# Performance work log

Measured on AMD Instinct MI355X. Metric: run time of the kernel, lower is better.

Reference implementation:

```python
import jax, jax.numpy as jnp
import numpy as np

E, T, D, H = 32, 65536, 512, 1024


def setup_inputs() -> dict:
    key = jax.random.key(0)
    k = jax.random.split(key, 7)
    norm = lambda kk, shp, sc: (jax.random.normal(kk, shp, jnp.float32) * sc)
    x = norm(k[0], (T, D), 1.0)
    w1 = norm(k[1], (E, D, H), D ** -0.5)   # per-expert up-proj (gate branch)
    b1 = norm(k[2], (E, H), 0.02)
    w3 = norm(k[3], (E, D, H), D ** -0.5)   # per-expert up-proj (linear branch)
    b3 = norm(k[4], (E, H), 0.02)
    w2 = norm(k[5], (E, H, D), H ** -0.5)   # per-expert down-proj
    b2 = norm(k[6], (E, D), 0.02)
    # tokens are pre-sorted by expert; uniform dispatch of T//E tokens per expert
    group_sizes = jnp.full((E,), T // E, jnp.int32)
    return dict(x=x, w1=w1, b1=b1, w3=w3, b3=b3, w2=w2, b2=b2,
                group_sizes=group_sizes)


def reference(x, w1, b1, w3, b3, w2, b2, group_sizes):
    # expert id per token, derived from contiguous group sizes
    bounds = jnp.cumsum(group_sizes)                       # [E]
    seg = jnp.searchsorted(bounds, jnp.arange(x.shape[0]), side='right')  # [T]
    # grouped GEMMs: per-expert weight bank applied to its contiguous token slab
    h1 = jax.lax.ragged_dot(x, w1, group_sizes) + b1[seg]  # [T,H]
    h3 = jax.lax.ragged_dot(x, w3, group_sizes) + b3[seg]  # [T,H]
    h = jax.nn.silu(h1) * h3                               # SwiGLU gate
    out = jax.lax.ragged_dot(h, w2, group_sizes) + b2[seg] # [T,D]
    return out
```

## Files before the change

### kernel.cpp

```cpp
#include <hip/hip_runtime.h>
#include <hip/hip_bf16.h>

#define TOK 65536
#define NE  32
#define DD  512
#define HH  1024
#define TPE 2048

typedef short s16x8  __attribute__((ext_vector_type(8)));
typedef float f32x16 __attribute__((ext_vector_type(16)));
using u16 = unsigned short;
using u32 = unsigned int;

__device__ __forceinline__ u16 f2bf(float f) {
  __bf16 h = (__bf16)f;
  return __builtin_bit_cast(u16, h);
}
__device__ __forceinline__ u32 pk2(float lo, float hi) {
  return (u32)f2bf(lo) | ((u32)f2bf(hi) << 16);
}
__device__ __forceinline__ int swz(int row, int colb) {
  return (row << 7) + (colb ^ ((row & 7) << 4));
}

#define MFMA(a, b, c) __builtin_amdgcn_mfma_f32_32x32x16_bf16(a, b, c, 0, 0, 0)
#define GLD(src, dst) __builtin_amdgcn_global_load_lds( \
    (const __attribute__((address_space(1))) void*)(src), \
    (__attribute__((address_space(3))) void*)(dst), 16, 0, 0)
#define SETP(n) __builtin_amdgcn_s_setprio(n)

__global__ __launch_bounds__(256) void p1_cvt_x(
    const float* __restrict__ x, u16* __restrict__ xb) {
  const size_t i = ((size_t)blockIdx.x * 256 + threadIdx.x) * 8;
  const float4 a = *(const float4*)(x + i);
  const float4 b = *(const float4*)(x + i + 4);
  uint4 v;
  v.x = pk2(a.x, a.y); v.y = pk2(a.z, a.w);
  v.z = pk2(b.x, b.y); v.w = pk2(b.z, b.w);
  *(uint4*)(xb + i) = v;
}

__global__ __launch_bounds__(256) void p2_w13t(
    const float* __restrict__ w1, const float* __restrict__ w3,
    u16* __restrict__ w13t) {
  __shared__ __align__(16) u16 L1[64 * 72], L3[64 * 72];
  const int bid = blockIdx.x;
  const int e = bid >> 7, rr = bid & 127;
  const int d0 = (rr & 7) << 6, h0 = (rr >> 3) << 6;
  const int t = threadIdx.x;
  const float* const s1 = w1 + (size_t)e * DD * HH + (size_t)d0 * HH + h0;
  const float* const s3 = w3 + (size_t)e * DD * HH + (size_t)d0 * HH + h0;
  const int cg = (t & 15) << 2, rbase = t >> 4;
#pragma unroll
  for (int j = 0; j < 4; ++j) {
    const int dr = rbase + (j << 4);
    const float4 a = *(const float4*)(s1 + (size_t)dr * HH + cg);
    const float4 b = *(const float4*)(s3 + (size_t)dr * HH + cg);
    L1[(cg + 0) * 72 + dr] = f2bf(a.x); L1[(cg + 1) * 72 + dr] = f2bf(a.y);
    L1[(cg + 2) * 72 + dr] = f2bf(a.z); L1[(cg + 3) * 72 + dr] = f2bf(a.w);
    L3[(cg + 0) * 72 + dr] = f2bf(b.x); L3[(cg + 1) * 72 + dr] = f2bf(b.y);
    L3[(cg + 2) * 72 + dr] = f2bf(b.z); L3[(cg + 3) * 72 + dr] = f2bf(b.w);
  }
  __syncthreads();
  u16* const dst = w13t + (size_t)e * (2 * HH) * DD;
  const int cb8 = (t & 7) << 3;
#pragma unroll
  for (int j = 0; j < 2; ++j) {
    const int nloc = (t >> 3) + (j << 5);
    const int n = h0 + nloc;
    const int R1 = ((n >> 5) << 6) + (n & 31);
    const uint4 v1 = *(const uint4*)(L1 + nloc * 72 + cb8);
    const uint4 v3 = *(const uint4*)(L3 + nloc * 72 + cb8);
    *(uint4*)(dst + (size_t)R1 * DD + d0 + cb8) = v1;
    *(uint4*)(dst + (size_t)(R1 + 32) * DD + d0 + cb8) = v3;
  }
}

__global__ __launch_bounds__(256) void p3_w2t(
    const float* __restrict__ w2, u16* __restrict__ w2t) {
  __shared__ __align__(16) u16 L[64 * 72];
  const int bid = blockIdx.x;
  const int e = bid >> 7, rr = bid & 127;
  const int d0 = (rr & 7) << 6, h0 = (rr >> 3) << 6;
  const int t = threadIdx.x;
  const float* const s = w2 + (size_t)e * HH * DD + (size_t)h0 * DD + d0;
  const int cg = (t & 15) << 2, rbase = t >> 4;
#pragma unroll
  for (int j = 0; j < 4; ++j) {
    const int hr = rbase + (j << 4);
    const float4 a = *(const float4*)(s + (size_t)hr * DD + cg);
    L[(cg + 0) * 72 + hr] = f2bf(a.x); L[(cg + 1) * 72 + hr] = f2bf(a.y);
    L[(cg + 2) * 72 + hr] = f2bf(a.z); L[(cg + 3) * 72 + hr] = f2bf(a.w);
  }
  __syncthreads();
  u16* const dst = w2t + (size_t)e * DD * HH;
  const int cb8 = (t & 7) << 3;
#pragma unroll
  for (int j = 0; j < 2; ++j) {
    const int dloc = (t >> 3) + (j << 5);
    const uint4 v = *(const uint4*)(L + dloc * 72 + cb8);
    *(uint4*)(dst + (size_t)(d0 + dloc) * HH + h0 + cb8) = v;
  }
}

template <int MODE>
__global__ __launch_bounds__(512, 2) void gemm256(
    const u16* __restrict__ A, const u16* __restrict__ Bm,
    const float* __restrict__ bx, const float* __restrict__ by,
    void* __restrict__ outp) {
  constexpr int K  = MODE ? HH : DD;
  constexpr int NT = K >> 6;
  constexpr int NB = MODE ? 2 : 8;
  __shared__ __align__(16) char lds[131072];

  const int bid = blockIdx.x;
  const int e   = bid / (8 * NB);
  const int rr  = bid % (8 * NB);
  const int m_t = rr & 7;
  const int n_t = rr >> 3;
  const int rowbase = e * TPE + (m_t << 8);

  const int t = threadIdx.x;
  const int wv = t >> 6, lane = t & 63;
  const int l31 = lane & 31, half = lane >> 5;
  const int wm = wv >> 2, wn = wv & 3;

  const u16* const Abase = A + (size_t)rowbase * K;
  const u16* const Bbase = Bm + ((size_t)e * NB + n_t) * 256 * K;

  int soff[4];
#pragma unroll
  for (int j = 0; j < 4; ++j) {
    const int c = (j << 9) + t;
    const int r = c >> 3, ci = c & 7;
    soff[j] = r * K + ((((ci << 4) ^ ((r & 7) << 4))) >> 1);
  }
  const int lbw = wv << 10;

  auto stage = [&](int kt, int buf) {
    char* const dA = lds + (buf << 16);
    char* const dB = dA + 32768;
    const u16* const Ak = Abase + (kt << 6);
    const u16* const Bk = Bbase + (kt << 6);
#pragma unroll
    for (int j = 0; j < 4; ++j) {
      GLD(Ak + soff[j], dA + (j << 13) + lbw);
      GLD(Bk + soff[j], dB + (j << 13) + lbw);
    }
  };

  const int swr = (l31 & 7) << 4;
  f32x16 acc[4][2] = {};
  s16x8 bb[2][2];

#define LDA(As, mf, ks) \
  (*(const s16x8*)((As) + (((wm << 7) + ((mf) << 5) + l31) << 7) + \
                   ((((ks) << 5) + (half << 4)) ^ swr)))
#define LDB(Bs, nf, ks) \
  (*(const s16x8*)((Bs) + (((wn << 6) + ((nf) << 5) + l31) << 7) + \
                   ((((ks) << 5) + (half << 4)) ^ swr)))
#define PH_B(Bs, kh) \
  bb[0][0] = LDB(Bs, 0, 2*(kh));     bb[0][1] = LDB(Bs, 1, 2*(kh)); \
  bb[1][0] = LDB(Bs, 0, 2*(kh)+1);   bb[1][1] = LDB(Bs, 1, 2*(kh)+1);
#define PH_AM(As, mh, kh) { \
  const s16x8 x0 = LDA(As, 2*(mh),   2*(kh)); \
  const s16x8 x1 = LDA(As, 2*(mh),   2*(kh)+1); \
  const s16x8 x2 = LDA(As, 2*(mh)+1, 2*(kh)); \
  const s16x8 x3 = LDA(As, 2*(mh)+1, 2*(kh)+1); \
  SETP(1); \
  acc[2*(mh)][0]   = MFMA(x0, bb[0][0], acc[2*(mh)][0]); \
  acc[2*(mh)][1]   = MFMA(x0, bb[0][1], acc[2*(mh)][1]); \
  acc[2*(mh)][0]   = MFMA(x1, bb[1][0], acc[2*(mh)][0]); \
  acc[2*(mh)][1]   = MFMA(x1, bb[1][1], acc[2*(mh)][1]); \
  acc[2*(mh)+1][0] = MFMA(x2, bb[0][0], acc[2*(mh)+1][0]); \
  acc[2*(mh)+1][1] = MFMA(x2, bb[0][1], acc[2*(mh)+1][1]); \
  acc[2*(mh)+1][0] = MFMA(x3, bb[1][0], acc[2*(mh)+1][0]); \
  acc[2*(mh)+1][1] = MFMA(x3, bb[1][1], acc[2*(mh)+1][1]); \
  SETP(0); }

  stage(0, 0);
  for (int kt = 0; kt < NT; ++kt) {
    const int cur = kt & 1;
    if (kt + 1 < NT) {
      stage(kt + 1, cur ^ 1);
      asm volatile("s_waitcnt vmcnt(8)" ::: "memory");
    } else {
      asm volatile("s_waitcnt vmcnt(0)" ::: "memory");
    }
    __builtin_amdgcn_s_barrier();
    __builtin_amdgcn_sched_barrier(0);
    {
      const char* const As = lds + (cur << 16);
      const char* const Bs = As + 32768;
      PH_B(Bs, 0);
      PH_AM(As, 0, 0);
      PH_AM(As, 1, 0);
      PH_B(Bs, 1);
      PH_AM(As, 0, 1);
      PH_AM(As, 1, 1);
    }
    asm volatile("s_waitcnt lgkmcnt(0)" ::: "memory");
    __builtin_amdgcn_sched_barrier(0);
    __builtin_amdgcn_s_barrier();
  }
#undef LDA
#undef LDB
#undef PH_B
#undef PH_AM

  if constexpr (MODE == 0) {
    const int g = (n_t << 2) + wn;
    const int hcol = (g << 5) + l31;
    const float bv1 = bx[e * HH + hcol];
    const float bv3 = by[e * HH + hcol];
    u16* const hp = (u16*)outp;
#pragma unroll
    for (int mf = 0; mf < 4; ++mf) {
#pragma unroll
      for (int rg = 0; rg < 16; ++rg) {
        const int grow = rowbase + (wm << 7) + (mf << 5) +
                         (rg & 3) + ((rg >> 2) << 3) + (half << 2);
        const float s1 = acc[mf][0][rg] + bv1;
        const float s3 = acc[mf][1][rg] + bv3;
        hp[(size_t)grow * HH + hcol] = f2bf(s1 * s3 / (1.0f + __expf(-s1)));
      }
    }
  } else {
    float* const op = (float*)outp;
#pragma unroll
    for (int mf = 0; mf < 4; ++mf) {
#pragma unroll
      for (int nf = 0; nf < 2; ++nf) {
        const int col = (n_t << 8) + (wn << 6) + (nf << 5) + l31;
        const float bv = bx[e * DD + col];
#pragma unroll
        for (int rg = 0; rg < 16; ++rg) {
          const int grow = rowbase + (wm << 7) + (mf << 5) +
                           (rg & 3) + ((rg >> 2) << 3) + (half << 2);
          op[(size_t)grow * DD + col] = acc[mf][nf][rg] + bv;
        }
      }
    }
  }
}

__global__ __launch_bounds__(256, 2) void k1_up_swiglu(
    const float* __restrict__ x,  const float* __restrict__ w1,
    const float* __restrict__ b1, const float* __restrict__ w3,
    const float* __restrict__ b3, u16* __restrict__ hbuf) {
  __shared__ __align__(16) char lds[32768];
  char* const As  = lds;
  char* const B1s = lds + 16384;
  char* const B3s = lds + 24576;
  const int bid = blockIdx.x;
  const int e = bid >> 8, rr = bid & 255;
  const int m_t = rr & 15, n_t = rr >> 4;
  const int rowbase = e * TPE + (m_t << 7), colbase = n_t << 6;
  const int t = threadIdx.x, wv = t >> 6, lane = t & 63;
  const int l31 = lane & 31, half = lane >> 5;
  const int wm = wv >> 1, wn = wv & 1;
  const int ag = t & 15, am0 = t >> 4, bn = t & 63, bk0 = t >> 6;
  const float* const xb = x + (size_t)rowbase * DD + (ag << 2);
  const size_t woff = (size_t)e * (DD * HH) + colbase + bn;
  const float* const w1b = w1 + woff;
  const float* const w3b = w3 + woff;
  float4 ra[8]; float rb1[16], rb3[16];
  auto gload = [&](int kt) {
    const float* xp = xb + (kt << 6);
#pragma unroll
    for (int j = 0; j < 8; ++j)
      ra[j] = *(const float4*)(xp + (size_t)(am0 + (j << 4)) * DD);
#pragma unroll
    for (int j = 0; j < 2; ++j) {
      const int k0 = (kt << 6) + ((bk0 + (j << 2)) << 3);
#pragma unroll
      for (int i = 0; i < 8; ++i) {
        rb1[(j << 3) + i] = w1b[(size_t)(k0 + i) * HH];
        rb3[(j << 3) + i] = w3b[(size_t)(k0 + i) * HH];
      }
    }
  };
  f32x16 acc10 = {}, acc11 = {}, acc30 = {}, acc31 = {};
  gload(0);
  for (int kt = 0; kt < 8; ++kt) {
    if (kt) __syncthreads();
#pragma unroll
    for (int j = 0; j < 8; ++j) {
      const int m = am0 + (j << 4);
      uint2 v; v.x = pk2(ra[j].x, ra[j].y); v.y = pk2(ra[j].z, ra[j].w);
      *(uint2*)(As + swz(m, ag << 3)) = v;
    }
#pragma unroll
    for (int j = 0; j < 2; ++j) {
      const int kg = bk0 + (j << 2);
      uint4 v;
      v.x = pk2(rb1[(j << 3) + 0], rb1[(j << 3) + 1]);
      v.y = pk2(rb1[(j << 3) + 2], rb1[(j << 3) + 3]);
      v.z = pk2(rb1[(j << 3) + 4], rb1[(j << 3) + 5]);
      v.w = pk2(rb1[(j << 3) + 6], rb1[(j << 3) + 7]);
      *(uint4*)(B1s + swz(bn, kg << 4)) = v;
      v.x = pk2(rb3[(j << 3) + 0], rb3[(j << 3) + 1]);
      v.y = pk2(rb3[(j << 3) + 2], rb3[(j << 3) + 3]);
      v.z = pk2(rb3[(j << 3) + 4], rb3[(j << 3) + 5]);
      v.w = pk2(rb3[(j << 3) + 6], rb3[(j << 3) + 7]);
      *(uint4*)(B3s + swz(bn, kg << 4)) = v;
    }
    __syncthreads();
    if (kt < 7) gload(kt + 1);
#pragma unroll
    for (int kk = 0; kk < 4; ++kk) {
      const int colb = (kk << 5) + (half << 4);
      const s16x8 a0 = *(const s16x8*)(As  + swz((wm << 6) + l31,      colb));
      const s16x8 a1 = *(const s16x8*)(As  + swz((wm << 6) + 32 + l31, colb));
      const s16x8 f1 = *(const s16x8*)(B1s + swz((wn << 5) + l31,      colb));
      const s16x8 f3 = *(const s16x8*)(B3s + swz((wn << 5) + l31,      colb));
      acc10 = MFMA(a0, f1, acc10); acc30 = MFMA(a0, f3, acc30);
      acc11 = MFMA(a1, f1, acc11); acc31 = MFMA(a1, f3, acc31);
    }
  }
  const int gcol = colbase + (wn << 5) + l31;
  const float bv1 = b1[e * HH + gcol], bv3 = b3[e * HH + gcol];
  u16* const hp = hbuf + gcol;
#pragma unroll
  for (int mb = 0; mb < 2; ++mb) {
    const f32x16 A1 = mb ? acc11 : acc10;
    const f32x16 A3 = mb ? acc31 : acc30;
#pragma unroll
    for (int rg = 0; rg < 16; ++rg) {
      const int grow = rowbase + (wm << 6) + (mb << 5) +
                       (rg & 3) + ((rg >> 2) << 3) + (half << 2);
      const float s1 = A1[rg] + bv1, s3 = A3[rg] + bv3;
      hp[(size_t)grow * HH] = f2bf(s1 * s3 / (1.0f + __expf(-s1)));
    }
  }
}

__global__ __launch_bounds__(256, 2) void k2_down(
    const u16* __restrict__ hbuf, const float* __restrict__ w2,
    const float* __restrict__ b2, float* __restrict__ out) {
  __shared__ __align__(16) char lds[32768];
  char* const As = lds;
  char* const Bs = lds + 16384;
  const int bid = blockIdx.x;
  const int e = bid >> 6, rr = bid & 63;
  const int m_t = rr & 15, n_t = rr >> 4;
  const int rowbase = e * TPE + (m_t << 7), colbase = n_t << 7;
  const int t = threadIdx.x, wv = t >> 6, lane = t & 63;
  const int l31 = lane & 31, half = lane >> 5;
  const int wm = wv >> 1, wn = wv & 1;
  const int ag = t & 7, am0 = t >> 3, bnn = t & 127, bk0 = t >> 7;
  const u16* const hb = hbuf + (size_t)rowbase * HH + (ag << 3);
  const float* const w2b = w2 + (size_t)e * (HH * DD) + colbase + bnn;
  uint4 ra[4]; float rb[32];
  auto gload = [&](int kt) {
#pragma unroll
    for (int j = 0; j < 4; ++j)
      ra[j] = *(const uint4*)(hb + (size_t)(am0 + (j << 5)) * HH + (kt << 6));
#pragma unroll
    for (int j = 0; j < 4; ++j) {
      const int k0 = (kt << 6) + ((bk0 + (j << 1)) << 3);
#pragma unroll
      for (int i = 0; i < 8; ++i)
        rb[(j << 3) + i] = w2b[(size_t)(k0 + i) * DD];
    }
  };
  f32x16 c00 = {}, c01 = {}, c10 = {}, c11 = {};
  gload(0);
  for (int kt = 0; kt < 16; ++kt) {
    if (kt) __syncthreads();
#pragma unroll
    for (int j = 0; j < 4; ++j)
      *(uint4*)(As + swz(am0 + (j << 5), ag << 4)) = ra[j];
#pragma unroll
    for (int j = 0; j < 4; ++j) {
      const int kg = bk0 + (j << 1);
      uint4 v;
      v.x = pk2(rb[(j << 3) + 0], rb[(j << 3) + 1]);
      v.y = pk2(rb[(j << 3) + 2], rb[(j << 3) + 3]);
      v.z = pk2(rb[(j << 3) + 4], rb[(j << 3) + 5]);
      v.w = pk2(rb[(j << 3) + 6], rb[(j << 3) + 7]);
      *(uint4*)(Bs + swz(bnn, kg << 4)) = v;
    }
    __syncthreads();
    if (kt < 15) gload(kt + 1);
#pragma unroll
    for (int kk = 0; kk < 4; ++kk) {
      const int colb = (kk << 5) + (half << 4);
      const s16x8 af0 = *(const s16x8*)(As + swz((wm << 6) + l31,      colb));
      const s16x8 af1 = *(const s16x8*)(As + swz((wm << 6) + 32 + l31, colb));
      const s16x8 bf0 = *(const s16x8*)(Bs + swz((wn << 6) + l31,      colb));
      const s16x8 bf1 = *(const s16x8*)(Bs + swz((wn << 6) + 32 + l31, colb));
      c00 = MFMA(af0, bf0, c00); c01 = MFMA(af0, bf1, c01);
      c10 = MFMA(af1, bf0, c10); c11 = MFMA(af1, bf1, c11);
    }
  }
#pragma unroll
  for (int mb = 0; mb < 2; ++mb) {
#pragma unroll
    for (int nb = 0; nb < 2; ++nb) {
      const f32x16 c = mb ? (nb ? c11 : c10) : (nb ? c01 : c00);
      const int gcol = colbase + (wn << 6) + (nb << 5) + l31;
      const float bv = b2[e * DD + gcol];
#pragma unroll
      for (int rg = 0; rg < 16; ++rg) {
        const int grow = rowbase + (wm << 6) + (mb << 5) +
                         (rg & 3) + ((rg >> 2) << 3) + (half << 2);
        out[(size_t)grow * DD + gcol] = c[rg] + bv;
      }
    }
  }
}

extern "C" void kernel_launch(void* const* d_in, const int* in_sizes, int n_in,
                              void* d_out, int out_size, void* d_ws, size_t ws_size,
                              hipStream_t stream) {
  const float* x  = (const float*)d_in[0];
  const float* w1 = (const float*)d_in[1];
  const float* b1 = (const float*)d_in[2];
  const float* w3 = (const float*)d_in[3];
  const float* b3 = (const float*)d_in[4];
  const float* w2 = (const float*)d_in[5];
  const float* b2 = (const float*)d_in[6];

  const size_t W13T_B = (size_t)NE * 2 * HH * DD * 2;
  const size_t W2T_B  = (size_t)NE * DD * HH * 2;
  const size_t H_B    = (size_t)TOK * HH * 2;

  if (ws_size >= W13T_B + W2T_B + H_B) {
    u16* const xb   = (u16*)d_out;
    u16* const w13t = (u16*)d_ws;
    u16* const w2t  = (u16*)((char*)d_ws + W13T_B);
    u16* const hbuf = (u16*)((char*)d_ws + W13T_B + W2T_B);

    p1_cvt_x<<<dim3(TOK * DD / 2048), dim3(256), 0, stream>>>(x, xb);
    p2_w13t <<<dim3(NE * 128),        dim3(256), 0, stream>>>(w1, w3, w13t);
    p3_w2t  <<<dim3(NE * 128),        dim3(256), 0, stream>>>(w2, w2t);
    gemm256<0><<<dim3(NE * 64), dim3(512), 0, stream>>>(xb, w13t, b1, b3, hbuf);
    gemm256<1><<<dim3(NE * 16), dim3(512), 0, stream>>>(hbuf, w2t, b2, nullptr, d_out);
  } else {
    u16* hbuf = (ws_size >= H_B) ? (u16*)d_ws : (u16*)d_out;
    k1_up_swiglu<<<dim3(NE * 256), dim3(256), 0, stream>>>(x, w1, b1, w3, b3, hbuf);
    k2_down<<<dim3(NE * 64), dim3(256), 0, stream>>>(hbuf, w2, b2, (float*)d_out);
  }
}
```

Baseline: 386.5 us.

## Split GEMM K-tile into four quarter-phases with interleaved staging and XCD block remap

```diff
diff --git a/kernel.cpp b/kernel.cpp
--- a/kernel.cpp
+++ b/kernel.cpp
@@ -28,6 +28,8 @@
     (const __attribute__((address_space(1))) void*)(src), \
     (__attribute__((address_space(3))) void*)(dst), 16, 0, 0)
 #define SETP(n) __builtin_amdgcn_s_setprio(n)
+#define SCHEDB() __builtin_amdgcn_sched_barrier(0)
+#define SBAR()  __builtin_amdgcn_s_barrier()
 
 __global__ __launch_bounds__(256) void p1_cvt_x(
     const float* __restrict__ x, u16* __restrict__ xb) {
@@ -104,16 +106,18 @@
 }
 
 template <int MODE>
-__global__ __launch_bounds__(512, 2) void gemm256(
+__global__ __launch_bounds__(512, 2) void gemm4p(
     const u16* __restrict__ A, const u16* __restrict__ Bm,
     const float* __restrict__ bx, const float* __restrict__ by,
     void* __restrict__ outp) {
   constexpr int K  = MODE ? HH : DD;
   constexpr int NT = K >> 6;
   constexpr int NB = MODE ? 2 : 8;
+  constexpr int NWG = NE * 8 * NB;
   __shared__ __align__(16) char lds[131072];
 
-  const int bid = blockIdx.x;
+  int bid = blockIdx.x;
+  bid = (bid & 7) * (NWG / 8) + (bid >> 3);
   const int e   = bid / (8 * NB);
   const int rr  = bid % (8 * NB);
   const int m_t = rr & 7;
@@ -128,85 +132,85 @@
   const u16* const Abase = A + (size_t)rowbase * K;
   const u16* const Bbase = Bm + ((size_t)e * NB + n_t) * 256 * K;
 
-  int soff[4];
-#pragma unroll
-  for (int j = 0; j < 4; ++j) {
-    const int c = (j << 9) + t;
-    const int r = c >> 3, ci = c & 7;
-    soff[j] = r * K + ((((ci << 4) ^ ((r & 7) << 4))) >> 1);
-  }
-  const int lbw = wv << 10;
-
-  auto stage = [&](int kt, int buf) {
-    char* const dA = lds + (buf << 16);
-    char* const dB = dA + 32768;
-    const u16* const Ak = Abase + (kt << 6);
-    const u16* const Bk = Bbase + (kt << 6);
-#pragma unroll
-    for (int j = 0; j < 4; ++j) {
-      GLD(Ak + soff[j], dA + (j << 13) + lbw);
-      GLD(Bk + soff[j], dB + (j << 13) + lbw);
-    }
+  int srcoff0, srcoff1;
+  {
+    const int c0 = t,       lr0 = c0 >> 3, s0 = (c0 & 7) ^ (lr0 & 7);
+    const int c1 = 512 + t, lr1 = c1 >> 3, s1 = (c1 & 7) ^ (lr1 & 7);
+    srcoff0 = ((lr0 << 1) | (s0 >> 2)) * K + ((s0 & 3) << 3);
+    srcoff1 = ((lr1 << 1) | (s1 >> 2)) * K + ((s1 & 3) << 3);
+  }
+  const int t16 = t << 4;
+
+  auto stageQ = [&](int tau, int q) {
+    const u16* const src = ((q & 1) ? Bbase : Abase) + tau * 64 + (q >> 1) * 32;
+    char* const dst = lds + ((tau & 1) << 16) + (q << 14);
+    GLD(src + srcoff0, dst + t16);
+    GLD(src + srcoff1, dst + 8192 + t16);
   };
 
-  const int swr = (l31 & 7) << 4;
+  const int lrow_off = l31 >> 1;
+  const int pbit = l31 & 1;
+  const int sw7 = lrow_off & 7;
+  const int sA0 = (((pbit << 2) | 0 | half) ^ sw7) << 4;
+  const int sA1 = (((pbit << 2) | 2 | half) ^ sw7) << 4;
+  const int aoff = ((wm << 6) + lrow_off) << 7;
+  const int boff = ((wn << 5) + lrow_off) << 7;
+
   f32x16 acc[4][2] = {};
-  s16x8 bb[2][2];
-
-#define LDA(As, mf, ks) \
-  (*(const s16x8*)((As) + (((wm << 7) + ((mf) << 5) + l31) << 7) + \
-                   ((((ks) << 5) + (half << 4)) ^ swr)))
-#define LDB(Bs, nf, ks) \
-  (*(const s16x8*)((Bs) + (((wn << 6) + ((nf) << 5) + l31) << 7) + \
-                   ((((ks) << 5) + (half << 4)) ^ swr)))
-#define PH_B(Bs, kh) \
-  bb[0][0] = LDB(Bs, 0, 2*(kh));     bb[0][1] = LDB(Bs, 1, 2*(kh)); \
-  bb[1][0] = LDB(Bs, 0, 2*(kh)+1);   bb[1][1] = LDB(Bs, 1, 2*(kh)+1);
-#define PH_AM(As, mh, kh) { \
-  const s16x8 x0 = LDA(As, 2*(mh),   2*(kh)); \
-  const s16x8 x1 = LDA(As, 2*(mh),   2*(kh)+1); \
-  const s16x8 x2 = LDA(As, 2*(mh)+1, 2*(kh)); \
-  const s16x8 x3 = LDA(As, 2*(mh)+1, 2*(kh)+1); \
-  SETP(1); \
-  acc[2*(mh)][0]   = MFMA(x0, bb[0][0], acc[2*(mh)][0]); \
-  acc[2*(mh)][1]   = MFMA(x0, bb[0][1], acc[2*(mh)][1]); \
-  acc[2*(mh)][0]   = MFMA(x1, bb[1][0], acc[2*(mh)][0]); \
-  acc[2*(mh)][1]   = MFMA(x1, bb[1][1], acc[2*(mh)][1]); \
-  acc[2*(mh)+1][0] = MFMA(x2, bb[0][0], acc[2*(mh)+1][0]); \
-  acc[2*(mh)+1][1] = MFMA(x2, bb[0][1], acc[2*(mh)+1][1]); \
-  acc[2*(mh)+1][0] = MFMA(x3, bb[1][0], acc[2*(mh)+1][0]); \
-  acc[2*(mh)+1][1] = MFMA(x3, bb[1][1], acc[2*(mh)+1][1]); \
-  SETP(0); }
-
-  stage(0, 0);
-  for (int kt = 0; kt < NT; ++kt) {
-    const int cur = kt & 1;
-    if (kt + 1 < NT) {
-      stage(kt + 1, cur ^ 1);
-      asm volatile("s_waitcnt vmcnt(8)" ::: "memory");
-    } else {
-      asm volatile("s_waitcnt vmcnt(0)" ::: "memory");
-    }
-    __builtin_amdgcn_s_barrier();
-    __builtin_amdgcn_sched_barrier(0);
-    {
-      const char* const As = lds + (cur << 16);
-      const char* const Bs = As + 32768;
-      PH_B(Bs, 0);
-      PH_AM(As, 0, 0);
-      PH_AM(As, 1, 0);
-      PH_B(Bs, 1);
-      PH_AM(As, 0, 1);
-      PH_AM(As, 1, 1);
-    }
-    asm volatile("s_waitcnt lgkmcnt(0)" ::: "memory");
-    __builtin_amdgcn_sched_barrier(0);
-    __builtin_amdgcn_s_barrier();
-  }
-#undef LDA
-#undef LDB
-#undef PH_B
-#undef PH_AM
+  s16x8 b00{}, b01{}, b10{}, b11{};
+
+#define VM6 asm volatile("s_waitcnt vmcnt(6)" ::: "memory")
+#define VM4 asm volatile("s_waitcnt vmcnt(4)" ::: "memory")
+#define VM0 asm volatile("s_waitcnt vmcnt(0)" ::: "memory")
+#define NOPV ((void)0)
+
+#define PHASE(T, KH, MH, DOB, STG, VM) do { \
+  STG; VM; \
+  SCHEDB(); SBAR(); SCHEDB(); \
+  { const char* const Aq = lds + (((T) & 1) << 16) + ((KH) << 15); \
+    const char* const Bq = Aq + 16384; \
+    if (DOB) { \
+      b00 = *(const s16x8*)(Bq + boff + 0 * 2048 + sA0); \
+      b01 = *(const s16x8*)(Bq + boff + 1 * 2048 + sA0); \
+      b10 = *(const s16x8*)(Bq + boff + 0 * 2048 + sA1); \
+      b11 = *(const s16x8*)(Bq + boff + 1 * 2048 + sA1); \
+    } \
+    const s16x8 a0 = *(const s16x8*)(Aq + aoff + (2 * (MH)) * 2048 + sA0); \
+    const s16x8 a1 = *(const s16x8*)(Aq + aoff + (2 * (MH)) * 2048 + sA1); \
+    const s16x8 a2 = *(const s16x8*)(Aq + aoff + (2 * (MH) + 1) * 2048 + sA0); \
+    const s16x8 a3 = *(const s16x8*)(Aq + aoff + (2 * (MH) + 1) * 2048 + sA1); \
+    SETP(1); \
+    acc[2 * (MH)][0]     = MFMA(a0, b00, acc[2 * (MH)][0]); \
+    acc[2 * (MH)][1]     = MFMA(a0, b01, acc[2 * (MH)][1]); \
+    acc[2 * (MH)][0]     = MFMA(a1, b10, acc[2 * (MH)][0]); \
+    acc[2 * (MH)][1]     = MFMA(a1, b11, acc[2 * (MH)][1]); \
+    acc[2 * (MH) + 1][0] = MFMA(a2, b00, acc[2 * (MH) + 1][0]); \
+    acc[2 * (MH) + 1][1] = MFMA(a2, b01, acc[2 * (MH) + 1][1]); \
+    acc[2 * (MH) + 1][0] = MFMA(a3, b10, acc[2 * (MH) + 1][0]); \
+    acc[2 * (MH) + 1][1] = MFMA(a3, b11, acc[2 * (MH) + 1][1]); \
+    SETP(0); \
+  } \
+} while (0)
+
+  stageQ(0, 0); stageQ(0, 1); stageQ(0, 2); stageQ(0, 3);
+
+#pragma unroll 2
+  for (int kt = 0; kt < NT - 1; ++kt) {
+    PHASE(kt, 0, 0, true,  stageQ(kt + 1, 0), VM6);
+    PHASE(kt, 0, 1, false, stageQ(kt + 1, 1), NOPV);
+    PHASE(kt, 1, 0, true,  stageQ(kt + 1, 2), VM6);
+    PHASE(kt, 1, 1, false, stageQ(kt + 1, 3), NOPV);
+  }
+  PHASE(NT - 1, 0, 0, true,  NOPV, VM4);
+  PHASE(NT - 1, 0, 1, false, NOPV, NOPV);
+  PHASE(NT - 1, 1, 0, true,  NOPV, VM0);
+  PHASE(NT - 1, 1, 1, false, NOPV, NOPV);
+
+#undef PHASE
+#undef VM6
+#undef VM4
+#undef VM0
+#undef NOPV
 
   if constexpr (MODE == 0) {
     const int g = (n_t << 2) + wn;
@@ -435,8 +439,8 @@
     p1_cvt_x<<<dim3(TOK * DD / 2048), dim3(256), 0, stream>>>(x, xb);
     p2_w13t <<<dim3(NE * 128),        dim3(256), 0, stream>>>(w1, w3, w13t);
     p3_w2t  <<<dim3(NE * 128),        dim3(256), 0, stream>>>(w2, w2t);
-    gemm256<0><<<dim3(NE * 64), dim3(512), 0, stream>>>(xb, w13t, b1, b3, hbuf);
-    gemm256<1><<<dim3(NE * 16), dim3(512), 0, stream>>>(hbuf, w2t, b2, nullptr, d_out);
+    gemm4p<0><<<dim3(NE * 64), dim3(512), 0, stream>>>(xb, w13t, b1, b3, hbuf);
+    gemm4p<1><<<dim3(NE * 16), dim3(512), 0, stream>>>(hbuf, w2t, b2, nullptr, d_out);
   } else {
     u16* hbuf = (ws_size >= H_B) ? (u16*)d_ws : (u16*)d_out;
     k1_up_swiglu<<<dim3(NE * 256), dim3(256), 0, stream>>>(x, w1, b1, w3, b3, hbuf);
```

After: 360.5 us. 1.07x faster.
